# Kernel tuning notes

Hardware: AMD Instinct MI355X
Metric: run time of the kernel (lower is better)

## Reference

```python
import jax, jax.numpy as jnp
import numpy as np

B, T, D, H = 2, 2048, 1024, 16
DK = D // H


def setup_inputs() -> dict:
    key = jax.random.key(0)
    ks = jax.random.split(key, 12)
    q = jax.random.normal(ks[0], (B, T, D), jnp.float32)
    k = jax.random.normal(ks[1], (B, T, D), jnp.float32)
    v = jax.random.normal(ks[2], (B, T, D), jnp.float32)
    # padding mask [B,1,T]: 1 = valid, 0 = pad (nonzero per torch eq(0) semantics)
    lengths = jnp.array([T, (3 * T) // 4])
    mask = (jnp.arange(T)[None, None, :] < lengths[:, None, None]).astype(jnp.int32)
    s = 0.02
    Wq = jax.random.normal(ks[3], (D, D), jnp.float32) * s
    Wk = jax.random.normal(ks[4], (D, D), jnp.float32) * s
    Wv = jax.random.normal(ks[5], (D, D), jnp.float32) * s
    Wo = jax.random.normal(ks[6], (D, D), jnp.float32) * s
    bq = jnp.zeros((D,), jnp.float32)
    bk = jnp.zeros((D,), jnp.float32)
    bv = jnp.zeros((D,), jnp.float32)
    bo = jnp.zeros((D,), jnp.float32)
    return {"query": q, "key": k, "value": v, "mask": mask,
            "Wq": Wq, "bq": bq, "Wk": Wk, "bk": bk,
            "Wv": Wv, "bv": bv, "Wo": Wo, "bo": bo}


def reference(query, key, value, mask, Wq, bq, Wk, bk, Wv, bv, Wo, bo):
    # q,k,v projections -> [B, H, T, DK]
    def proj(x, W, b):
        return (x @ W.T + b).reshape(B, T, H, DK).transpose(0, 2, 1, 3)
    q = proj(query, Wq, bq)
    k = proj(key, Wk, bk)
    v = proj(value, Wv, bv)
    scores = jnp.einsum("bhqd,bhkd->bhqk", q, k) * (DK ** -0.5)  # [B,H,T,T]
    m = (mask == 0)[:, None, :, :]  # [B,1,1,T] broadcast over heads/queries
    scores = jnp.where(m, -jnp.inf, scores)
    attn = jax.nn.softmax(scores, axis=-1)
    attn = jnp.where(m, 0.0, attn)
    x = jnp.einsum("bhqk,bhkd->bhqd", attn, v)  # [B,H,T,DK]
    x = x.transpose(0, 2, 1, 3).reshape(B, T, D)
    return x @ Wo.T + bo
```

## Files before the change

kernel.cpp:

```cpp
#include <hip/hip_runtime.h>

typedef unsigned short u16;
typedef unsigned int u32;
typedef __bf16 bf16x8 __attribute__((ext_vector_type(8)));
typedef float floatx4 __attribute__((ext_vector_type(4)));

#define BB 2
#define TT 2048
#define DD 1024
#define HH 16
#define DKK 64
#define ACT (BB * TT * DD)
#define WTE (DD * DD)

__device__ inline u16 f2bf(float f) {
    union { float f; u32 u; } c; c.f = f;
    u32 r = (c.u + 0x7fffu + ((c.u >> 16) & 1u)) >> 16;
    return (u16)r;
}
__device__ inline u32 pack2bf(float a, float b) {
    return (u32)f2bf(a) | ((u32)f2bf(b) << 16);
}

typedef __attribute__((address_space(1))) const u32 gas_u32;
typedef __attribute__((address_space(3))) u32 las_u32;
__device__ __forceinline__ void gl2lds16(const u16* g, u16* l) {
    __builtin_amdgcn_global_load_lds((gas_u32*)g, (las_u32*)l, 16, 0, 0);
}

__device__ __forceinline__ u32 cvtpk_bf16(float lo, float hi) {
    u32 r;
    asm("v_cvt_pk_bf16_f32 %0, %1, %2" : "=v"(r) : "v"(lo), "v"(hi));
    return r;
}

__device__ __forceinline__ void quad_gather(u32 &a, u32 &b) {
    asm volatile("s_nop 1\n\t"
                 "v_permlane32_swap_b32 %0, %1\n\t"
                 "s_nop 1\n\t"
                 "v_permlane16_swap_b32 %0, %1"
                 : "+v"(a), "+v"(b));
}

struct CvtArgs { const float* src[7]; u16* dst[7]; };
__global__ __launch_bounds__(256) void convert_bf16(CvtArgs a) {
    int bid = blockIdx.x, t, local;
    if (bid < 768) { t = bid >> 8; local = bid & 255; }
    else { int r = bid - 768; t = 3 + (r >> 6); local = r & 63; }
    const float* s = a.src[t];
    u16* d = a.dst[t];
    const int base = local * 16384;
    for (int i = 0; i < 8; i++) {
        const int idx = base + i * 2048 + threadIdx.x * 8;
        float4 x0 = *(const float4*)(s + idx);
        float4 x1 = *(const float4*)(s + idx + 4);
        uint4 p;
        p.x = pack2bf(x0.x, x0.y); p.y = pack2bf(x0.z, x0.w);
        p.z = pack2bf(x1.x, x1.y); p.w = pack2bf(x1.z, x1.w);
        *(uint4*)(d + idx) = p;
    }
}

__global__ __launch_bounds__(256) void qkv_gemm(
    const u16* __restrict__ Qc, const u16* __restrict__ Kc,
    const u16* __restrict__ Vc,
    const u16* __restrict__ Wqc, const u16* __restrict__ Wkc,
    const u16* __restrict__ Wvc,
    const float* __restrict__ bq, const float* __restrict__ bk,
    const float* __restrict__ bv,
    u16* __restrict__ ws)
{
    __shared__ __align__(16) u16 As[128 * 32];
    __shared__ __align__(16) u16 Bs[128 * 32];
    const int z = blockIdx.z;
    const u16* A = (z == 0) ? Qc : (z == 1) ? Kc : Vc;
    const u16* W = (z == 0) ? Wqc : (z == 1) ? Wkc : Wvc;
    const float* bias = (z == 0) ? bq : (z == 1) ? bk : bv;
    u16* out = ws + (size_t)z * (size_t)BB * HH * TT * DKK;

    const int tid  = threadIdx.x;
    const int wave = tid >> 6, lane = tid & 63;
    const int quad = lane >> 4, l16 = lane & 15;
    const int wm = wave & 1, wn = wave >> 1;
    const int m0 = blockIdx.y * 128, n0 = blockIdx.x * 128;
    const int K = DD;

    const int lrow = lane >> 2, lcol = (lane & 3) * 8;
    const u16* Ag0 = A + (size_t)(m0 + wave * 16 + lrow) * K + lcol;
    const u16* Ag1 = A + (size_t)(m0 + 64 + wave * 16 + lrow) * K + lcol;
    const u16* Wg0 = W + (size_t)(n0 + wave * 16 + lrow) * K + lcol;
    const u16* Wg1 = W + (size_t)(n0 + 64 + wave * 16 + lrow) * K + lcol;
    u16* AsD0 = &As[(wave * 16) * 32];
    u16* AsD1 = &As[(64 + wave * 16) * 32];
    u16* BsD0 = &Bs[(wave * 16) * 32];
    u16* BsD1 = &Bs[(64 + wave * 16) * 32];

    floatx4 acc[4][4];
    for (int i = 0; i < 4; i++)
        for (int j = 0; j < 4; j++)
            acc[i][j] = floatx4{0.f, 0.f, 0.f, 0.f};

    for (int k0 = 0; k0 < K; k0 += 32) {
        __syncthreads();
        gl2lds16(Ag0 + k0, AsD0);
        gl2lds16(Ag1 + k0, AsD1);
        gl2lds16(Wg0 + k0, BsD0);
        gl2lds16(Wg1 + k0, BsD1);
        __syncthreads();

        bf16x8 af[4], bfr[4];
        for (int mi = 0; mi < 4; mi++)
            af[mi] = *(const bf16x8*)&As[(wm * 64 + mi * 16 + l16) * 32 + quad * 8];
        for (int ni = 0; ni < 4; ni++)
            bfr[ni] = *(const bf16x8*)&Bs[(wn * 64 + ni * 16 + l16) * 32 + quad * 8];
        for (int mi = 0; mi < 4; mi++)
            for (int ni = 0; ni < 4; ni++)
                acc[mi][ni] = __builtin_amdgcn_mfma_f32_16x16x32_bf16(
                    af[mi], bfr[ni], acc[mi][ni], 0, 0, 0);
    }

    for (int ni = 0; ni < 4; ni++) {
        const int n = n0 + wn * 64 + ni * 16 + l16;
        const float bv2 = bias[n];
        for (int mi = 0; mi < 4; mi++) {
            for (int vv = 0; vv < 4; vv++) {
                const int m = m0 + wm * 64 + mi * 16 + quad * 4 + vv;
                const float val = acc[mi][ni][vv] + bv2;
                const int b = m >> 11, t = m & 2047, h = n >> 6, dk = n & 63;
                if (z == 2)
                    out[(((size_t)(b * HH + h)) * DKK + dk) * TT + t] = f2bf(val);
                else
                    out[(((size_t)(b * HH + h)) * TT + t) * DKK + dk] = f2bf(val);
            }
        }
    }
}

__global__ __launch_bounds__(256) void out_gemm(
    const u16* __restrict__ Av, const u16* __restrict__ Wv,
    const float* __restrict__ bias, float* __restrict__ outv)
{
    __shared__ __align__(16) u16 As[128 * 32];
    __shared__ __align__(16) u16 Bs[128 * 32];
    const int tid  = threadIdx.x;
    const int wave = tid >> 6, lane = tid & 63;
    const int quad = lane >> 4, l16 = lane & 15;
    const int wm = wave & 1, wn = wave >> 1;
    const int m0 = blockIdx.y * 128, n0 = blockIdx.x * 128;
    const int K = DD, N = DD;

    const int lrow = lane >> 2, lcol = (lane & 3) * 8;
    const u16* Ag0 = Av + (size_t)(m0 + wave * 16 + lrow) * K + lcol;
    const u16* Ag1 = Av + (size_t)(m0 + 64 + wave * 16 + lrow) * K + lcol;
    const u16* Wg0 = Wv + (size_t)(n0 + wave * 16 + lrow) * K + lcol;
    const u16* Wg1 = Wv + (size_t)(n0 + 64 + wave * 16 + lrow) * K + lcol;
    u16* AsD0 = &As[(wave * 16) * 32];
    u16* AsD1 = &As[(64 + wave * 16) * 32];
    u16* BsD0 = &Bs[(wave * 16) * 32];
    u16* BsD1 = &Bs[(64 + wave * 16) * 32];

    floatx4 acc[4][4];
    for (int i = 0; i < 4; i++)
        for (int j = 0; j < 4; j++)
            acc[i][j] = floatx4{0.f, 0.f, 0.f, 0.f};

    for (int k0 = 0; k0 < K; k0 += 32) {
        __syncthreads();
        gl2lds16(Ag0 + k0, AsD0);
        gl2lds16(Ag1 + k0, AsD1);
        gl2lds16(Wg0 + k0, BsD0);
        gl2lds16(Wg1 + k0, BsD1);
        __syncthreads();

        bf16x8 af[4], bfr[4];
        for (int mi = 0; mi < 4; mi++)
            af[mi] = *(const bf16x8*)&As[(wm * 64 + mi * 16 + l16) * 32 + quad * 8];
        for (int ni = 0; ni < 4; ni++)
            bfr[ni] = *(const bf16x8*)&Bs[(wn * 64 + ni * 16 + l16) * 32 + quad * 8];
        for (int mi = 0; mi < 4; mi++)
            for (int ni = 0; ni < 4; ni++)
                acc[mi][ni] = __builtin_amdgcn_mfma_f32_16x16x32_bf16(
                    af[mi], bfr[ni], acc[mi][ni], 0, 0, 0);
    }

    for (int ni = 0; ni < 4; ni++) {
        const int n = n0 + wn * 64 + ni * 16 + l16;
        const float bv2 = bias[n];
        for (int mi = 0; mi < 4; mi++)
            for (int vv = 0; vv < 4; vv++) {
                const int m = m0 + wm * 64 + mi * 16 + quad * 4 + vv;
                outv[(size_t)m * N + n] = acc[mi][ni][vv] + bv2;
            }
    }
}

__global__ __launch_bounds__(512) void attn_kernel(
    const u16* __restrict__ Qp, const u16* __restrict__ Kp,
    const u16* __restrict__ Vpt, const int* __restrict__ mask,
    u16* __restrict__ Xa)
{
    constexpr int LDK = 72;
    __shared__ __align__(16) u16 Ks[64 * LDK];
    __shared__ __align__(16) u16 Vs[64 * LDK];
    const int tid  = threadIdx.x;
    const int wave = tid >> 6, lane = tid & 63;
    const int quad = lane >> 4, l16 = lane & 15;
    const int bid = blockIdx.x;
    const int qt = bid & 15, bh = bid >> 4;
    const int b = bh >> 4, h = bh & 15;
    const int qbase = qt * 128 + wave * 16;

    const u16* Qb = Qp + (size_t)bh * TT * DKK;
    const u16* Kb = Kp + (size_t)bh * TT * DKK;
    const u16* Vb = Vpt + (size_t)bh * DKK * TT;
    const int* mk = mask + b * TT;

    const int srow = tid >> 3, scol = (tid & 7) * 8;

    const bf16x8 qf0 = *(const bf16x8*)&Qb[(size_t)(qbase + l16) * DKK + quad * 8];
    const bf16x8 qf1 = *(const bf16x8*)&Qb[(size_t)(qbase + l16) * DKK + 32 + quad * 8];

    floatx4 o[4];
    for (int i = 0; i < 4; i++) o[i] = floatx4{0.f, 0.f, 0.f, 0.f};
    float rs = 0.f;

    uint4 kr = *(const uint4*)&Kb[(size_t)srow * DKK + scol];
    uint4 vr = *(const uint4*)&Vb[(size_t)srow * TT + scol];

    for (int ti = 0; ti < TT / 64; ti++) {
        const int k0 = ti * 64;
        __syncthreads();
        *(uint4*)&Ks[srow * LDK + scol] = kr;
        *(uint4*)&Vs[srow * LDK + scol] = vr;
        __syncthreads();
        if (ti + 1 < TT / 64) {
            kr = *(const uint4*)&Kb[(size_t)(k0 + 64 + srow) * DKK + scol];
            vr = *(const uint4*)&Vb[(size_t)srow * TT + k0 + 64 + scol];
        }

        const int mv0 = mk[k0 + l16];
        const int mv1 = mk[k0 + 16 + l16];
        const int mv2 = mk[k0 + 32 + l16];
        const int mv3 = mk[k0 + 48 + l16];
        if (!__any(mv0 | mv1 | mv2 | mv3)) continue;
        const bool allv = __all(mv0 && mv1 && mv2 && mv3);

        bf16x8 kf[4][2];
        #pragma unroll
        for (int c = 0; c < 4; c++) {
            kf[c][0] = *(const bf16x8*)&Ks[(c * 16 + l16) * LDK + quad * 8];
            kf[c][1] = *(const bf16x8*)&Ks[(c * 16 + l16) * LDK + 32 + quad * 8];
        }

        floatx4 s[4];
        #pragma unroll
        for (int c = 0; c < 4; c++) s[c] = floatx4{0.f, 0.f, 0.f, 0.f};
        #pragma unroll
        for (int c = 0; c < 4; c++) {
            s[c] = __builtin_amdgcn_mfma_f32_16x16x32_bf16(kf[c][0], qf0, s[c], 0, 0, 0);
            s[c] = __builtin_amdgcn_mfma_f32_16x16x32_bf16(kf[c][1], qf1, s[c], 0, 0, 0);
        }

        float p[4][4];
        if (allv) {
            #pragma unroll
            for (int c = 0; c < 4; c++)
                #pragma unroll
                for (int v = 0; v < 4; v++)
                    p[c][v] = __expf(s[c][v] * 0.125f);
        } else {
            #pragma unroll
            for (int c = 0; c < 4; c++)
                #pragma unroll
                for (int v = 0; v < 4; v++)
                    p[c][v] = mk[k0 + c * 16 + quad * 4 + v]
                                  ? __expf(s[c][v] * 0.125f) : 0.f;
        }
        #pragma unroll
        for (int c = 0; c < 4; c++)
            #pragma unroll
            for (int v = 0; v < 4; v++)
                rs += p[c][v];

        u32 A0 = cvtpk_bf16(p[0][0], p[0][1]), B0 = cvtpk_bf16(p[1][0], p[1][1]);
        u32 A1 = cvtpk_bf16(p[0][2], p[0][3]), B1 = cvtpk_bf16(p[1][2], p[1][3]);
        u32 A2 = cvtpk_bf16(p[2][0], p[2][1]), B2 = cvtpk_bf16(p[3][0], p[3][1]);
        u32 A3 = cvtpk_bf16(p[2][2], p[2][3]), B3 = cvtpk_bf16(p[3][2], p[3][3]);
        quad_gather(A0, B0);
        quad_gather(A1, B1);
        quad_gather(A2, B2);
        quad_gather(A3, B3);
        union { u32 w[4]; bf16x8 v; } pa0, pa1;
        pa0.w[0] = A0; pa0.w[1] = A1; pa0.w[2] = B0; pa0.w[3] = B1;
        pa1.w[0] = A2; pa1.w[1] = A3; pa1.w[2] = B2; pa1.w[3] = B3;

        #pragma unroll
        for (int nb = 0; nb < 4; nb++) {
            const bf16x8 vf0 = *(const bf16x8*)&Vs[(nb * 16 + l16) * LDK + quad * 8];
            const bf16x8 vf1 = *(const bf16x8*)&Vs[(nb * 16 + l16) * LDK + 32 + quad * 8];
            o[nb] = __builtin_amdgcn_mfma_f32_16x16x32_bf16(pa0.v, vf0, o[nb], 0, 0, 0);
            o[nb] = __builtin_amdgcn_mfma_f32_16x16x32_bf16(pa1.v, vf1, o[nb], 0, 0, 0);
        }
    }

    rs += __shfl_xor(rs, 16, 64);
    rs += __shfl_xor(rs, 32, 64);
    float inv[4];
    #pragma unroll
    for (int v = 0; v < 4; v++)
        inv[v] = 1.0f / __shfl(rs, quad * 4 + v, 64);

    #pragma unroll
    for (int nb = 0; nb < 4; nb++)
        #pragma unroll
        for (int v = 0; v < 4; v++) {
            const int t = qbase + quad * 4 + v;
            Xa[((size_t)b * TT + t) * DD + h * DKK + nb * 16 + l16] =
                f2bf(o[nb][v] * inv[v]);
        }
}

extern "C" void kernel_launch(void* const* d_in, const int* in_sizes, int n_in,
                              void* d_out, int out_size, void* d_ws, size_t ws_size,
                              hipStream_t stream) {
    const float* q    = (const float*)d_in[0];
    const float* k    = (const float*)d_in[1];
    const float* v    = (const float*)d_in[2];
    const int*   mask = (const int*)d_in[3];
    const float* Wq   = (const float*)d_in[4];
    const float* bq   = (const float*)d_in[5];
    const float* Wk   = (const float*)d_in[6];
    const float* bk   = (const float*)d_in[7];
    const float* Wv   = (const float*)d_in[8];
    const float* bv   = (const float*)d_in[9];
    const float* Wo   = (const float*)d_in[10];
    const float* bo   = (const float*)d_in[11];

    u16* Qc  = (u16*)d_ws;
    u16* Kc  = Qc + (size_t)ACT;
    u16* Vc  = Kc + (size_t)ACT;
    u16* Wqc = Vc + (size_t)ACT;
    u16* Wkc = Wqc + (size_t)WTE;
    u16* Wvc = Wkc + (size_t)WTE;
    u16* Woc = Wvc + (size_t)WTE;
    u16* Qp  = Woc + (size_t)WTE;
    u16* Kp  = Qp + (size_t)ACT;
    u16* Vpt = Kp + (size_t)ACT;
    u16* Xa  = Vpt + (size_t)ACT;

    CvtArgs ca;
    ca.src[0] = q;  ca.dst[0] = Qc;
    ca.src[1] = k;  ca.dst[1] = Kc;
    ca.src[2] = v;  ca.dst[2] = Vc;
    ca.src[3] = Wq; ca.dst[3] = Wqc;
    ca.src[4] = Wk; ca.dst[4] = Wkc;
    ca.src[5] = Wv; ca.dst[5] = Wvc;
    ca.src[6] = Wo; ca.dst[6] = Woc;
    convert_bf16<<<1024, 256, 0, stream>>>(ca);

    qkv_gemm<<<dim3(DD / 128, (BB * TT) / 128, 3), 256, 0, stream>>>(
        Qc, Kc, Vc, Wqc, Wkc, Wvc, bq, bk, bv, Qp);

    attn_kernel<<<dim3(BB * HH * (TT / 128)), 512, 0, stream>>>(Qp, Kp, Vpt, mask, Xa);

    out_gemm<<<dim3(DD / 128, (BB * TT) / 128), 256, 0, stream>>>(Xa, Woc, bo, (float*)d_out);
}
```

Before: 236.6 us.

## Give each attention wave two 16-row query blocks, halving block size

The attention kernel now launches 256 threads (4 waves) per block instead of 512. Each wave handles 32 query rows as two 16-row MFMA blocks, so every K/V fragment read from LDS feeds twice as many MFMAs. Each thread now stages two K and two V vectors per tile. This cuts LDS fragment reads and barrier overhead per unit of compute, at the cost of more registers per thread and fewer waves available to hide latency.

```diff
diff --git a/kernel.cpp b/kernel.cpp
--- a/kernel.cpp
+++ b/kernel.cpp
@@ -194,7 +194,7 @@
     }
 }
 
-__global__ __launch_bounds__(512) void attn_kernel(
+__global__ __launch_bounds__(256) void attn_kernel(
     const u16* __restrict__ Qp, const u16* __restrict__ Kp,
     const u16* __restrict__ Vpt, const int* __restrict__ mask,
     u16* __restrict__ Xa)
@@ -208,7 +208,7 @@
     const int bid = blockIdx.x;
     const int qt = bid & 15, bh = bid >> 4;
     const int b = bh >> 4, h = bh & 15;
-    const int qbase = qt * 128 + wave * 16;
+    const int qbase = qt * 128 + wave * 32;
 
     const u16* Qb = Qp + (size_t)bh * TT * DKK;
     const u16* Kb = Kp + (size_t)bh * TT * DKK;
@@ -217,25 +217,37 @@
 
     const int srow = tid >> 3, scol = (tid & 7) * 8;
 
-    const bf16x8 qf0 = *(const bf16x8*)&Qb[(size_t)(qbase + l16) * DKK + quad * 8];
-    const bf16x8 qf1 = *(const bf16x8*)&Qb[(size_t)(qbase + l16) * DKK + 32 + quad * 8];
-
-    floatx4 o[4];
-    for (int i = 0; i < 4; i++) o[i] = floatx4{0.f, 0.f, 0.f, 0.f};
-    float rs = 0.f;
-
-    uint4 kr = *(const uint4*)&Kb[(size_t)srow * DKK + scol];
-    uint4 vr = *(const uint4*)&Vb[(size_t)srow * TT + scol];
+    bf16x8 qf[2][2];
+    #pragma unroll
+    for (int mb = 0; mb < 2; mb++) {
+        qf[mb][0] = *(const bf16x8*)&Qb[(size_t)(qbase + mb * 16 + l16) * DKK + quad * 8];
+        qf[mb][1] = *(const bf16x8*)&Qb[(size_t)(qbase + mb * 16 + l16) * DKK + 32 + quad * 8];
+    }
+
+    floatx4 o[2][4];
+    float rs[2] = {0.f, 0.f};
+    for (int mb = 0; mb < 2; mb++)
+        for (int i = 0; i < 4; i++)
+            o[mb][i] = floatx4{0.f, 0.f, 0.f, 0.f};
+
+    uint4 kr0 = *(const uint4*)&Kb[(size_t)srow * DKK + scol];
+    uint4 kr1 = *(const uint4*)&Kb[(size_t)(32 + srow) * DKK + scol];
+    uint4 vr0 = *(const uint4*)&Vb[(size_t)srow * TT + scol];
+    uint4 vr1 = *(const uint4*)&Vb[(size_t)(32 + srow) * TT + scol];
 
     for (int ti = 0; ti < TT / 64; ti++) {
         const int k0 = ti * 64;
         __syncthreads();
-        *(uint4*)&Ks[srow * LDK + scol] = kr;
-        *(uint4*)&Vs[srow * LDK + scol] = vr;
+        *(uint4*)&Ks[srow * LDK + scol] = kr0;
+        *(uint4*)&Ks[(32 + srow) * LDK + scol] = kr1;
+        *(uint4*)&Vs[srow * LDK + scol] = vr0;
+        *(uint4*)&Vs[(32 + srow) * LDK + scol] = vr1;
         __syncthreads();
         if (ti + 1 < TT / 64) {
-            kr = *(const uint4*)&Kb[(size_t)(k0 + 64 + srow) * DKK + scol];
-            vr = *(const uint4*)&Vb[(size_t)srow * TT + k0 + 64 + scol];
+            kr0 = *(const uint4*)&Kb[(size_t)(k0 + 64 + srow) * DKK + scol];
+            kr1 = *(const uint4*)&Kb[(size_t)(k0 + 96 + srow) * DKK + scol];
+            vr0 = *(const uint4*)&Vb[(size_t)srow * TT + k0 + 64 + scol];
+            vr1 = *(const uint4*)&Vb[(size_t)(32 + srow) * TT + k0 + 64 + scol];
         }
 
         const int mv0 = mk[k0 + l16];
@@ -252,72 +264,82 @@
             kf[c][1] = *(const bf16x8*)&Ks[(c * 16 + l16) * LDK + 32 + quad * 8];
         }
 
-        floatx4 s[4];
-        #pragma unroll
-        for (int c = 0; c < 4; c++) s[c] = floatx4{0.f, 0.f, 0.f, 0.f};
-        #pragma unroll
-        for (int c = 0; c < 4; c++) {
-            s[c] = __builtin_amdgcn_mfma_f32_16x16x32_bf16(kf[c][0], qf0, s[c], 0, 0, 0);
-            s[c] = __builtin_amdgcn_mfma_f32_16x16x32_bf16(kf[c][1], qf1, s[c], 0, 0, 0);
-        }
-
-        float p[4][4];
-        if (allv) {
+        union { u32 w[4]; bf16x8 v; } pa[2][2];
+        #pragma unroll
+        for (int mb = 0; mb < 2; mb++) {
+            floatx4 s[4];
+            #pragma unroll
+            for (int c = 0; c < 4; c++) s[c] = floatx4{0.f, 0.f, 0.f, 0.f};
+            #pragma unroll
+            for (int c = 0; c < 4; c++) {
+                s[c] = __builtin_amdgcn_mfma_f32_16x16x32_bf16(kf[c][0], qf[mb][0], s[c], 0, 0, 0);
+                s[c] = __builtin_amdgcn_mfma_f32_16x16x32_bf16(kf[c][1], qf[mb][1], s[c], 0, 0, 0);
+            }
+
+            float p[4][4];
+            if (allv) {
+                #pragma unroll
+                for (int c = 0; c < 4; c++)
+                    #pragma unroll
+                    for (int v = 0; v < 4; v++)
+                        p[c][v] = __expf(s[c][v] * 0.125f);
+            } else {
+                #pragma unroll
+                for (int c = 0; c < 4; c++)
+                    #pragma unroll
+                    for (int v = 0; v < 4; v++)
+                        p[c][v] = mk[k0 + c * 16 + quad * 4 + v]
+                                      ? __expf(s[c][v] * 0.125f) : 0.f;
+            }
             #pragma unroll
             for (int c = 0; c < 4; c++)
                 #pragma unroll
                 for (int v = 0; v < 4; v++)
-                    p[c][v] = __expf(s[c][v] * 0.125f);
-        } else {
-            #pragma unroll
-            for (int c = 0; c < 4; c++)
-                #pragma unroll
-                for (int v = 0; v < 4; v++)
-                    p[c][v] = mk[k0 + c * 16 + quad * 4 + v]
-                                  ? __expf(s[c][v] * 0.125f) : 0.f;
-        }
-        #pragma unroll
-        for (int c = 0; c < 4; c++)
-            #pragma unroll
-            for (int v = 0; v < 4; v++)
-                rs += p[c][v];
-
-        u32 A0 = cvtpk_bf16(p[0][0], p[0][1]), B0 = cvtpk_bf16(p[1][0], p[1][1]);
-        u32 A1 = cvtpk_bf16(p[0][2], p[0][3]), B1 = cvtpk_bf16(p[1][2], p[1][3]);
-        u32 A2 = cvtpk_bf16(p[2][0], p[2][1]), B2 = cvtpk_bf16(p[3][0], p[3][1]);
-        u32 A3 = cvtpk_bf16(p[2][2], p[2][3]), B3 = cvtpk_bf16(p[3][2], p[3][3]);
-        quad_gather(A0, B0);
-        quad_gather(A1, B1);
-        quad_gather(A2, B2);
-        quad_gather(A3, B3);
-        union { u32 w[4]; bf16x8 v; } pa0, pa1;
-        pa0.w[0] = A0; pa0.w[1] = A1; pa0.w[2] = B0; pa0.w[3] = B1;
-        pa1.w[0] = A2; pa1.w[1] = A3; pa1.w[2] = B2; pa1.w[3] = B3;
+                    rs[mb] += p[c][v];
+
+            u32 A0 = cvtpk_bf16(p[0][0], p[0][1]), B0 = cvtpk_bf16(p[1][0], p[1][1]);
+            u32 A1 = cvtpk_bf16(p[0][2], p[0][3]), B1 = cvtpk_bf16(p[1][2], p[1][3]);
+            u32 A2 = cvtpk_bf16(p[2][0], p[2][1]), B2 = cvtpk_bf16(p[3][0], p[3][1]);
+            u32 A3 = cvtpk_bf16(p[2][2], p[2][3]), B3 = cvtpk_bf16(p[3][2], p[3][3]);
+            quad_gather(A0, B0);
+            quad_gather(A1, B1);
+            quad_gather(A2, B2);
+            quad_gather(A3, B3);
+            pa[mb][0].w[0] = A0; pa[mb][0].w[1] = A1; pa[mb][0].w[2] = B0; pa[mb][0].w[3] = B1;
+            pa[mb][1].w[0] = A2; pa[mb][1].w[1] = A3; pa[mb][1].w[2] = B2; pa[mb][1].w[3] = B3;
+        }
 
         #pragma unroll
         for (int nb = 0; nb < 4; nb++) {
             const bf16x8 vf0 = *(const bf16x8*)&Vs[(nb * 16 + l16) * LDK + quad * 8];
             const bf16x8 vf1 = *(const bf16x8*)&Vs[(nb * 16 + l16) * LDK + 32 + quad * 8];
-            o[nb] = __builtin_amdgcn_mfma_f32_16x16x32_bf16(pa0.v, vf0, o[nb], 0, 0, 0);
-            o[nb] = __builtin_amdgcn_mfma_f32_16x16x32_bf16(pa1.v, vf1, o[nb], 0, 0, 0);
-        }
-    }
-
-    rs += __shfl_xor(rs, 16, 64);
-    rs += __shfl_xor(rs, 32, 64);
-    float inv[4];
+            o[0][nb] = __builtin_amdgcn_mfma_f32_16x16x32_bf16(pa[0][0].v, vf0, o[0][nb], 0, 0, 0);
+            o[0][nb] = __builtin_amdgcn_mfma_f32_16x16x32_bf16(pa[0][1].v, vf1, o[0][nb], 0, 0, 0);
+            o[1][nb] = __builtin_amdgcn_mfma_f32_16x16x32_bf16(pa[1][0].v, vf0, o[1][nb], 0, 0, 0);
+            o[1][nb] = __builtin_amdgcn_mfma_f32_16x16x32_bf16(pa[1][1].v, vf1, o[1][nb], 0, 0, 0);
+        }
+    }
+
+    float inv[2][4];
     #pragma unroll
-    for (int v = 0; v < 4; v++)
-        inv[v] = 1.0f / __shfl(rs, quad * 4 + v, 64);
+    for (int mb = 0; mb < 2; mb++) {
+        rs[mb] += __shfl_xor(rs[mb], 16, 64);
+        rs[mb] += __shfl_xor(rs[mb], 32, 64);
+        #pragma unroll
+        for (int v = 0; v < 4; v++)
+            inv[mb][v] = 1.0f / __shfl(rs[mb], quad * 4 + v, 64);
+    }
 
     #pragma unroll
-    for (int nb = 0; nb < 4; nb++)
-        #pragma unroll
-        for (int v = 0; v < 4; v++) {
-            const int t = qbase + quad * 4 + v;
-            Xa[((size_t)b * TT + t) * DD + h * DKK + nb * 16 + l16] =
-                f2bf(o[nb][v] * inv[v]);
-        }
+    for (int mb = 0; mb < 2; mb++)
+        #pragma unroll
+        for (int nb = 0; nb < 4; nb++)
+            #pragma unroll
+            for (int v = 0; v < 4; v++) {
+                const int t = qbase + mb * 16 + quad * 4 + v;
+                Xa[((size_t)b * TT + t) * DD + h * DKK + nb * 16 + l16] =
+                    f2bf(o[mb][nb][v] * inv[mb][v]);
+            }
 }
 
 extern "C" void kernel_launch(void* const* d_in, const int* in_sizes, int n_in,
@@ -361,7 +383,7 @@
     qkv_gemm<<<dim3(DD / 128, (BB * TT) / 128, 3), 256, 0, stream>>>(
         Qc, Kc, Vc, Wqc, Wkc, Wvc, bq, bk, bv, Qp);
 
-    attn_kernel<<<dim3(BB * HH * (TT / 128)), 512, 0, stream>>>(Qp, Kp, Vpt, mask, Xa);
+    attn_kernel<<<dim3(BB * HH * (TT / 128)), 256, 0, stream>>>(Qp, Kp, Vpt, mask, Xa);
 
     out_gemm<<<dim3(DD / 128, (BB * TT) / 128), 256, 0, stream>>>(Xa, Woc, bo, (float*)d_out);
 }
```

New measurement: 242.0 us. +2.3%, slower.
